# Kernel optimization log

Measured on AMD Instinct MI355X. Metric: run time of the kernel, lower is better.

The kernel has to match this reference:

```python
import jax, jax.numpy as jnp
import numpy as np


def gcn_layer(x, W, b, src, dst):
    """PyG GCNConv with improved=True: A_hat = A + 2I, D^-1/2 A_hat D^-1/2 X W + b."""
    n = x.shape[0]
    xw = x @ W  # [N, H]
    # degree counts each incoming edge (weight 1) plus self-loop weight 2
    deg = jnp.zeros((n,), x.dtype).at[dst].add(jnp.ones((src.shape[0],), x.dtype)) + 2.0
    dinv = jax.lax.rsqrt(deg)  # deg >= 2 always
    norm = (dinv[src] * dinv[dst])[:, None]  # [E, 1]
    agg = jax.ops.segment_sum(xw[src] * norm, dst, num_segments=n)  # scatter-add to dst
    agg = agg + (2.0 * dinv * dinv)[:, None] * xw  # self-loop contribution (weight 2)
    return agg + b


def xavier(k, shape):
    lim = (6.0 / (shape[0] + shape[1])) ** 0.5
    return jax.random.uniform(k, shape, jnp.float32, -lim, lim)


def setup_inputs() -> dict:
    key = jax.random.key(0)
    ks = jax.random.split(key, 8)
    N, E, D = 100_000, 1_600_000, 64  # nodes, edges, features_dim
    H1, H2 = 64, 64                   # gnn_dims
    M1, M2 = 128, 64                  # ind_pol_dims
    rep = jax.random.normal(ks[0], (N, D), jnp.float32)
    edge_index = jax.random.randint(ks[1], (2, E), 0, N, jnp.int32)
    return {
        "rep": rep,
        "edge_index": edge_index,
        "W1": xavier(ks[2], (D, H1)), "b1": jnp.zeros((H1,), jnp.float32),
        "W2": xavier(ks[3], (H1, H2)), "b2": jnp.zeros((H2,), jnp.float32),
        "Wa": xavier(ks[4], (H2 + D, M1)), "ba": jnp.zeros((M1,), jnp.float32),
        "Wb": xavier(ks[5], (M1, M2)), "bb": jnp.zeros((M2,), jnp.float32),
        "Wo": xavier(ks[6], (M2, 1)), "bo": jnp.zeros((1,), jnp.float32),
    }


def reference(rep, edge_index, W1, b1, W2, b2, Wa, ba, Wb, bb, Wo, bo):
    src, dst = edge_index[0], edge_index[1]
    # eval mode: f.dropout(training=False) is identity
    h = jax.nn.relu(gcn_layer(rep, W1, b1, src, dst))
    h = jax.nn.relu(gcn_layer(h, W2, b2, src, dst))
    z = jnp.concatenate([rep, h], axis=1)  # [N, D + H2]
    z = jax.nn.relu(z @ Wa + ba)
    z = jax.nn.relu(z @ Wb + bb)
    prob = jax.nn.sigmoid(z @ Wo + bo)[:, 0]  # [N]
    # gumbel_softmax(hard=True, tau=1) over logits = [1-p, p] (torch semantics:
    # probabilities fed directly as logits, as in the original code)
    logits = jnp.stack([1.0 - prob, prob], axis=1)  # [N, 2]
    u = jax.random.uniform(jax.random.key(42), logits.shape, jnp.float32, 1e-20, 1.0)
    g = -jnp.log(-jnp.log(u))
    y = jax.nn.softmax(logits + g, axis=1)
    hard = jax.nn.one_hot(jnp.argmax(y, axis=1), 2, dtype=y.dtype)
    st = hard + y - jax.lax.stop_gradient(y)  # straight-through
    ind = st @ jnp.array([[0.0], [1.0]], dtype=y.dtype)  # mm with [[0],[1]]
    return (prob, ind[:, 0])
```

## Files before the change

kernel.cpp:

```cpp
#include <hip/hip_runtime.h>
#include <math.h>


__device__ __forceinline__ unsigned rotl32(unsigned x, int r) {
  return (x << r) | (x >> (32 - r));
}

__device__ __forceinline__ void threefry2x32(unsigned k0, unsigned k1,
                                             unsigned x0, unsigned x1,
                                             unsigned& o0, unsigned& o1) {
  unsigned ks2 = k0 ^ k1 ^ 0x1BD11BDAu;
#define TF_RND(r) { x0 += x1; x1 = rotl32(x1, (r)); x1 ^= x0; }
  x0 += k0; x1 += k1;
  TF_RND(13) TF_RND(15) TF_RND(26) TF_RND(6)
  x0 += k1; x1 += ks2 + 1u;
  TF_RND(17) TF_RND(29) TF_RND(16) TF_RND(24)
  x0 += ks2; x1 += k0 + 2u;
  TF_RND(13) TF_RND(15) TF_RND(26) TF_RND(6)
  x0 += k0; x1 += k1 + 3u;
  TF_RND(17) TF_RND(29) TF_RND(16) TF_RND(24)
  x0 += k1; x1 += ks2 + 4u;
  TF_RND(13) TF_RND(15) TF_RND(26) TF_RND(6)
  x0 += ks2; x1 += k0 + 5u;
#undef TF_RND
  o0 = x0; o1 = x1;
}

__device__ __forceinline__ unsigned jax_random_bits_u32(unsigned k0, unsigned k1,
                                                        unsigned flat_idx) {
  unsigned a, b;
  threefry2x32(k0, k1, 0u, flat_idx, a, b);
  return a ^ b;
}

#define BSHIFT 8
#define BMASK 255

__global__ __launch_bounds__(256) void coarse_hist_kernel(
    const int* __restrict__ dst, int* __restrict__ coarse, int E) {
  __shared__ int h[512];
  for (int i = threadIdx.x; i < 512; i += 256) h[i] = 0;
  __syncthreads();
  for (int e = blockIdx.x * blockDim.x + threadIdx.x; e < E;
       e += gridDim.x * blockDim.x)
    atomicAdd(&h[dst[e] >> BSHIFT], 1);
  __syncthreads();
  for (int i = threadIdx.x; i < 512; i += 256)
    if (h[i]) atomicAdd(&coarse[i], h[i]);
}

__global__ __launch_bounds__(512) void coarse_scan_kernel(
    const int* __restrict__ coarse, int* __restrict__ bbase,
    int* __restrict__ cbase, int NBUCK) {
  __shared__ int sh[512];
  int t = threadIdx.x;
  int v = (t < NBUCK) ? coarse[t] : 0;
  sh[t] = v;
  __syncthreads();
  for (int o = 1; o < 512; o <<= 1) {
    int a = (t >= o) ? sh[t - o] : 0;
    __syncthreads();
    sh[t] += a;
    __syncthreads();
  }
  if (t < NBUCK) {
    int ex = sh[t] - v;
    bbase[t] = ex;
    cbase[t] = ex;
    if (t == NBUCK - 1) bbase[NBUCK] = sh[t];
  }
}

#define CHUNK 4096
__global__ __launch_bounds__(256) void scatter_gemm_kernel(
    const int* __restrict__ src, const int* __restrict__ dst,
    int* __restrict__ cbase, int* __restrict__ pkB, int E, int nbA,
    const float* __restrict__ X, const float* __restrict__ W,
    float* __restrict__ Y, int N) {
  __shared__ int smem[9216];
  const int t = threadIdx.x;

  if (blockIdx.x < nbA) {
    int* sS = smem;
    int* dS = smem + 4096;
    int* cnt = smem + 8192;
    int* base = smem + 8704;
    const int e0 = blockIdx.x * CHUNK;
    const int n = min(CHUNK, E - e0);
    for (int i = t; i < 512; i += 256) cnt[i] = 0;
    for (int i = t; i < n; i += 256) {
      sS[i] = src[e0 + i];
      dS[i] = dst[e0 + i];
    }
    __syncthreads();
    for (int i = t; i < n; i += 256) atomicAdd(&cnt[dS[i] >> BSHIFT], 1);
    __syncthreads();
    for (int i = t; i < 512; i += 256) {
      int c = cnt[i];
      base[i] = c ? atomicAdd(&cbase[i], c) : 0;
    }
    __syncthreads();
    for (int i = t; i < 512; i += 256) cnt[i] = 0;
    __syncthreads();
    for (int i = t; i < n; i += 256) {
      int d = dS[i];
      int b = d >> BSHIFT;
      int r = atomicAdd(&cnt[b], 1);
      pkB[base[b] + r] = ((d & BMASK) << 20) | sS[i];
    }
    return;
  }

  float* Ws = (float*)smem;
  float* Xs = (float*)smem + 4096;
  {
    const float4* W4 = (const float4*)W;
    float4* Ws4 = (float4*)Ws;
    for (int i = t; i < 1024; i += 256) Ws4[i] = W4[i];
  }
  const int row0 = (blockIdx.x - nbA) * 64;
  for (int i = t; i < 64 * 16; i += 256) {
    int r = i >> 4, c4 = i & 15;
    int gr = row0 + r;
    float4 v = make_float4(0.f, 0.f, 0.f, 0.f);
    if (gr < N) v = *(const float4*)&X[(size_t)gr * 64 + c4 * 4];
    *(float4*)&Xs[r * 68 + c4 * 4] = v;
  }
  __syncthreads();

  const int tx = t & 15, ty = t >> 4;
  const int c0 = tx * 4;
  const int r0 = ty * 4;
  float acc[4][4];
#pragma unroll
  for (int i = 0; i < 4; ++i)
#pragma unroll
    for (int j = 0; j < 4; ++j) acc[i][j] = 0.f;

#pragma unroll 4
  for (int k4 = 0; k4 < 16; ++k4) {
    float4 xv[4];
#pragma unroll
    for (int i = 0; i < 4; ++i)
      xv[i] = *(const float4*)&Xs[(r0 + i) * 68 + k4 * 4];
#pragma unroll
    for (int kk = 0; kk < 4; ++kk) {
      float w[4];
#pragma unroll
      for (int j = 0; j < 4; ++j) w[j] = Ws[(k4 * 4 + kk) * 64 + c0 + j];
      const float xk[4] = {
          kk == 0 ? xv[0].x : kk == 1 ? xv[0].y : kk == 2 ? xv[0].z : xv[0].w,
          kk == 0 ? xv[1].x : kk == 1 ? xv[1].y : kk == 2 ? xv[1].z : xv[1].w,
          kk == 0 ? xv[2].x : kk == 1 ? xv[2].y : kk == 2 ? xv[2].z : xv[2].w,
          kk == 0 ? xv[3].x : kk == 1 ? xv[3].y : kk == 2 ? xv[3].z : xv[3].w};
#pragma unroll
      for (int i = 0; i < 4; ++i)
#pragma unroll
        for (int j = 0; j < 4; ++j) acc[i][j] = fmaf(xk[i], w[j], acc[i][j]);
    }
  }

#pragma unroll
  for (int i = 0; i < 4; ++i) {
    int gr = row0 + r0 + i;
    if (gr >= N) continue;
    float4 v = make_float4(acc[i][0], acc[i][1], acc[i][2], acc[i][3]);
    *(float4*)&Y[(size_t)gr * 64 + c0] = v;
  }
}

__global__ __launch_bounds__(256) void bucket_finalize_kernel(
    const int* __restrict__ pkB, const int* __restrict__ bbase,
    int* __restrict__ off, float* __restrict__ dinv, int* __restrict__ srcS,
    int N) {
  __shared__ int cnt[256];
  __shared__ int sh[256];
  const int t = threadIdx.x;
  const int b = blockIdx.x;
  const int lo = bbase[b], hi = bbase[b + 1];
  cnt[t] = 0;
  __syncthreads();
  for (int i = lo + t; i < hi; i += 256) atomicAdd(&cnt[pkB[i] >> 20], 1);
  __syncthreads();
  const int deg = cnt[t];
  sh[t] = deg;
  __syncthreads();
  for (int o = 1; o < 256; o <<= 1) {
    int a = (t >= o) ? sh[t - o] : 0;
    __syncthreads();
    sh[t] += a;
    __syncthreads();
  }
  const int ex = sh[t] - deg;
  const int node = (b << BSHIFT) + t;
  if (node < N) {
    off[node] = lo + ex;
    dinv[node] = 1.0f / sqrtf((float)deg + 2.0f);
    if (node == N - 1) off[N] = hi;
  }
  cnt[t] = lo + ex;
  __syncthreads();
  for (int i = lo + t; i < hi; i += 256) {
    int u = pkB[i];
    int pos = atomicAdd(&cnt[u >> 20], 1);
    srcS[pos] = u & 0xFFFFF;
  }
}

__global__ __launch_bounds__(256) void aggregate_kernel(
    const float* __restrict__ xws, const int* __restrict__ srcS,
    const int* __restrict__ off, const float* __restrict__ dinv,
    const float* __restrict__ dinvS, const float* __restrict__ bias,
    float* __restrict__ h, int N) {
  int node = (blockIdx.x * blockDim.x + threadIdx.x) >> 6;
  int lane = threadIdx.x & 63;
  int g = lane >> 4;
  int fq = lane & 15;
  if (node >= N) return;
  const float4* xw4 = (const float4*)xws;
  int beg = off[node], end = off[node + 1];
  float4 a0 = make_float4(0.f, 0.f, 0.f, 0.f);
  float4 a1 = a0, a2 = a0, a3 = a0;
  if (dinvS) {
    for (int e = beg; e < end; e += 16) {
      int e0 = e + g, e1 = e + 4 + g, e2 = e + 8 + g, e3 = e + 12 + g;
      int s0 = srcS[min(e0, end - 1)];
      int s1 = srcS[min(e1, end - 1)];
      int s2 = srcS[min(e2, end - 1)];
      int s3 = srcS[min(e3, end - 1)];
      float d0 = dinvS[s0], d1 = dinvS[s1], d2 = dinvS[s2], d3 = dinvS[s3];
      float4 v0 = xw4[(size_t)s0 * 16 + fq];
      float4 v1 = xw4[(size_t)s1 * 16 + fq];
      float4 v2 = xw4[(size_t)s2 * 16 + fq];
      float4 v3 = xw4[(size_t)s3 * 16 + fq];
      if (e0 < end) { a0.x += d0*v0.x; a0.y += d0*v0.y; a0.z += d0*v0.z; a0.w += d0*v0.w; }
      if (e1 < end) { a1.x += d1*v1.x; a1.y += d1*v1.y; a1.z += d1*v1.z; a1.w += d1*v1.w; }
      if (e2 < end) { a2.x += d2*v2.x; a2.y += d2*v2.y; a2.z += d2*v2.z; a2.w += d2*v2.w; }
      if (e3 < end) { a3.x += d3*v3.x; a3.y += d3*v3.y; a3.z += d3*v3.z; a3.w += d3*v3.w; }
    }
  } else {
    for (int e = beg; e < end; e += 16) {
      int e0 = e + g, e1 = e + 4 + g, e2 = e + 8 + g, e3 = e + 12 + g;
      int s0 = srcS[min(e0, end - 1)];
      int s1 = srcS[min(e1, end - 1)];
      int s2 = srcS[min(e2, end - 1)];
      int s3 = srcS[min(e3, end - 1)];
      float4 v0 = xw4[(size_t)s0 * 16 + fq];
      float4 v1 = xw4[(size_t)s1 * 16 + fq];
      float4 v2 = xw4[(size_t)s2 * 16 + fq];
      float4 v3 = xw4[(size_t)s3 * 16 + fq];
      if (e0 < end) { a0.x += v0.x; a0.y += v0.y; a0.z += v0.z; a0.w += v0.w; }
      if (e1 < end) { a1.x += v1.x; a1.y += v1.y; a1.z += v1.z; a1.w += v1.w; }
      if (e2 < end) { a2.x += v2.x; a2.y += v2.y; a2.z += v2.z; a2.w += v2.w; }
      if (e3 < end) { a3.x += v3.x; a3.y += v3.y; a3.z += v3.z; a3.w += v3.w; }
    }
  }
  float4 a;
  a.x = (a0.x + a1.x) + (a2.x + a3.x);
  a.y = (a0.y + a1.y) + (a2.y + a3.y);
  a.z = (a0.z + a1.z) + (a2.z + a3.z);
  a.w = (a0.w + a1.w) + (a2.w + a3.w);
  a.x += __shfl_xor(a.x, 16, 64); a.x += __shfl_xor(a.x, 32, 64);
  a.y += __shfl_xor(a.y, 16, 64); a.y += __shfl_xor(a.y, 32, 64);
  a.z += __shfl_xor(a.z, 16, 64); a.z += __shfl_xor(a.z, 32, 64);
  a.w += __shfl_xor(a.w, 16, 64); a.w += __shfl_xor(a.w, 32, 64);
  if (g == 0) {
    float di = dinv[node];
    float4 self = xw4[(size_t)node * 16 + fq];
    if (dinvS) { self.x *= di; self.y *= di; self.z *= di; self.w *= di; }
    float4 b = ((const float4*)bias)[fq];
    float4 r;
    r.x = fmaxf(di * (a.x + 2.0f * self.x) + b.x, 0.f);
    r.y = fmaxf(di * (a.y + 2.0f * self.y) + b.y, 0.f);
    r.z = fmaxf(di * (a.z + 2.0f * self.z) + b.z, 0.f);
    r.w = fmaxf(di * (a.w + 2.0f * self.w) + b.w, 0.f);
    *(float4*)&h[(size_t)node * 64 + fq * 4] = r;
  }
}

__global__ __launch_bounds__(256) void gemm64v2_kernel(
    const float* __restrict__ X, const float* __restrict__ W,
    const float* __restrict__ dinv, float* __restrict__ Y, int N) {
  __shared__ float Ws[64 * 64];
  __shared__ float Xs[64 * 68];
  const int t = threadIdx.x;
  {
    const float4* W4 = (const float4*)W;
    float4* Ws4 = (float4*)Ws;
    for (int i = t; i < 16 * 64; i += 256) Ws4[i] = W4[i];
  }
  const int row0 = blockIdx.x * 64;
  for (int i = t; i < 64 * 16; i += 256) {
    int r = i >> 4, c4 = i & 15;
    int gr = row0 + r;
    float4 v = make_float4(0.f, 0.f, 0.f, 0.f);
    if (gr < N) v = *(const float4*)&X[(size_t)gr * 64 + c4 * 4];
    *(float4*)&Xs[r * 68 + c4 * 4] = v;
  }
  __syncthreads();

  const int tx = t & 15, ty = t >> 4;
  const int c0 = tx * 4;
  const int r0 = ty * 4;
  float acc[4][4];
#pragma unroll
  for (int i = 0; i < 4; ++i)
#pragma unroll
    for (int j = 0; j < 4; ++j) acc[i][j] = 0.f;

#pragma unroll 4
  for (int k4 = 0; k4 < 16; ++k4) {
    float4 xv[4];
#pragma unroll
    for (int i = 0; i < 4; ++i)
      xv[i] = *(const float4*)&Xs[(r0 + i) * 68 + k4 * 4];
#pragma unroll
    for (int kk = 0; kk < 4; ++kk) {
      float w[4];
#pragma unroll
      for (int j = 0; j < 4; ++j) w[j] = Ws[(k4 * 4 + kk) * 64 + c0 + j];
      const float xk[4] = {
          kk == 0 ? xv[0].x : kk == 1 ? xv[0].y : kk == 2 ? xv[0].z : xv[0].w,
          kk == 0 ? xv[1].x : kk == 1 ? xv[1].y : kk == 2 ? xv[1].z : xv[1].w,
          kk == 0 ? xv[2].x : kk == 1 ? xv[2].y : kk == 2 ? xv[2].z : xv[2].w,
          kk == 0 ? xv[3].x : kk == 1 ? xv[3].y : kk == 2 ? xv[3].z : xv[3].w};
#pragma unroll
      for (int i = 0; i < 4; ++i)
#pragma unroll
        for (int j = 0; j < 4; ++j) acc[i][j] = fmaf(xk[i], w[j], acc[i][j]);
    }
  }

#pragma unroll
  for (int i = 0; i < 4; ++i) {
    int gr = row0 + r0 + i;
    if (gr >= N) continue;
    float sc = dinv[gr];
    float4 v = make_float4(acc[i][0] * sc, acc[i][1] * sc, acc[i][2] * sc,
                           acc[i][3] * sc);
    *(float4*)&Y[(size_t)gr * 64 + c0] = v;
  }
}

__global__ __launch_bounds__(256) void head_mega_kernel(
    const float* __restrict__ rep, const float* __restrict__ h2,
    const float* __restrict__ Wa, const float* __restrict__ ba,
    const float* __restrict__ Wb, const float* __restrict__ bb,
    const float* __restrict__ Wo, const float* __restrict__ bo,
    float* __restrict__ out, int N) {
  __shared__ float Xs[64 * 128];
  __shared__ float Wbuf[32 * 128];
  const int t = threadIdx.x;
  const int row0 = blockIdx.x * 64;

  for (int i = t; i < 2048; i += 256) {
    int r = i >> 5, c4 = i & 31;
    int gr = row0 + r;
    float4 v = make_float4(0.f, 0.f, 0.f, 0.f);
    if (gr < N)
      v = (c4 < 16) ? *(const float4*)&rep[(size_t)gr * 64 + c4 * 4]
                    : *(const float4*)&h2[(size_t)gr * 64 + (c4 - 16) * 4];
    int scol = (c4 * 4 + ((r >> 2) << 2)) & 127;
    *(float4*)&Xs[r * 128 + scol] = v;
  }

  const int tx = t & 15, ty = t >> 4;
  const int cL = tx * 4;
  const int cH = 64 + tx * 4;
  const int r0 = ty * 4;
  float za[4][8];
#pragma unroll
  for (int i = 0; i < 4; ++i)
#pragma unroll
    for (int j = 0; j < 8; ++j) za[i][j] = 0.f;

  for (int chunk = 0; chunk < 4; ++chunk) {
    __syncthreads();
    const float4* Wa4 = (const float4*)(Wa + chunk * 32 * 128);
    float4* Wd = (float4*)Wbuf;
    for (int i = t; i < 1024; i += 256) Wd[i] = Wa4[i];
    __syncthreads();
    const int kb = chunk * 32;
#pragma unroll 2
    for (int kk = 0; kk < 32; ++kk) {
      const int kc = (kb + kk + (ty << 2)) & 127;
      float x[4];
#pragma unroll
      for (int i = 0; i < 4; ++i) x[i] = Xs[(r0 + i) * 128 + kc];
      float4 w0 = *(const float4*)&Wbuf[kk * 128 + cL];
      float4 w1 = *(const float4*)&Wbuf[kk * 128 + cH];
      const float w[8] = {w0.x, w0.y, w0.z, w0.w, w1.x, w1.y, w1.z, w1.w};
#pragma unroll
      for (int i = 0; i < 4; ++i)
#pragma unroll
        for (int j = 0; j < 8; ++j) za[i][j] = fmaf(x[i], w[j], za[i][j]);
    }
  }
#pragma unroll
  for (int i = 0; i < 4; ++i) {
#pragma unroll
    for (int j = 0; j < 4; ++j) {
      za[i][j] = fmaxf(za[i][j] + ba[cL + j], 0.f);
      za[i][4 + j] = fmaxf(za[i][4 + j] + ba[cH + j], 0.f);
    }
  }

  __syncthreads();
  float* zaS = Xs;
  {
    int sL = (cL + (ty << 2)) & 127;
    int sH = (cH + (ty << 2)) & 127;
#pragma unroll
    for (int i = 0; i < 4; ++i) {
      *(float4*)&zaS[(r0 + i) * 128 + sL] =
          make_float4(za[i][0], za[i][1], za[i][2], za[i][3]);
      *(float4*)&zaS[(r0 + i) * 128 + sH] =
          make_float4(za[i][4], za[i][5], za[i][6], za[i][7]);
    }
  }

  const int c0b = tx * 4;
  float zb[4][4];
#pragma unroll
  for (int i = 0; i < 4; ++i)
#pragma unroll
    for (int j = 0; j < 4; ++j) zb[i][j] = 0.f;

  for (int chunk = 0; chunk < 2; ++chunk) {
    __syncthreads();
    const float4* Wb4 = (const float4*)(Wb + chunk * 64 * 64);
    float4* Wd = (float4*)Wbuf;
    for (int i = t; i < 1024; i += 256) Wd[i] = Wb4[i];
    __syncthreads();
    const int kb = chunk * 64;
#pragma unroll 4
    for (int kk = 0; kk < 64; ++kk) {
      const int kc = (kb + kk + (ty << 2)) & 127;
      float x[4];
#pragma unroll
      for (int i = 0; i < 4; ++i) x[i] = zaS[(r0 + i) * 128 + kc];
      float4 w = *(const float4*)&Wbuf[kk * 64 + c0b];
      const float wj[4] = {w.x, w.y, w.z, w.w};
#pragma unroll
      for (int i = 0; i < 4; ++i)
#pragma unroll
        for (int j = 0; j < 4; ++j) zb[i][j] = fmaf(x[i], wj[j], zb[i][j]);
    }
  }
  float part[4];
#pragma unroll
  for (int i = 0; i < 4; ++i) {
    part[i] = 0.f;
#pragma unroll
    for (int j = 0; j < 4; ++j) {
      float v = fmaxf(zb[i][j] + bb[c0b + j], 0.f);
      part[i] = fmaf(v, Wo[c0b + j], part[i]);
    }
  }
  __syncthreads();
  float* red = Wbuf;
#pragma unroll
  for (int i = 0; i < 4; ++i) red[tx * 68 + r0 + i] = part[i];
  __syncthreads();
  if (t < 64) {
    int gr = row0 + t;
    if (gr < N) {
      float s = 0.f;
#pragma unroll
      for (int u = 0; u < 16; ++u) s += red[u * 68 + t];
      float w = s + bo[0];
      float p = 1.0f / (1.0f + expf(-w));
      unsigned i = (unsigned)gr;
      unsigned bits0 = jax_random_bits_u32(0u, 42u, 2u * i);
      unsigned bits1 = jax_random_bits_u32(0u, 42u, 2u * i + 1u);
      float f0 = __uint_as_float((bits0 >> 9) | 0x3f800000u) - 1.0f;
      float f1 = __uint_as_float((bits1 >> 9) | 0x3f800000u) - 1.0f;
      float u0 = fmaxf(1e-20f, f0 + 1e-20f);
      float u1 = fmaxf(1e-20f, f1 + 1e-20f);
      float g0 = -logf(-logf(u0));
      float g1 = -logf(-logf(u1));
      float a0 = (1.0f - p) + g0;
      float a1 = p + g1;
      float m = fmaxf(a0, a1);
      float e0 = expf(a0 - m), e1 = expf(a1 - m);
      float ssum = e0 + e1;
      float y0 = e0 / ssum, y1 = e1 / ssum;
      float hard1 = (y1 > y0) ? 1.0f : 0.0f;
      float st1 = (hard1 + y1) - y1;
      out[gr] = p;
      out[N + gr] = st1;
    }
  }
}

extern "C" void kernel_launch(void* const* d_in, const int* in_sizes, int n_in,
                              void* d_out, int out_size, void* d_ws, size_t ws_size,
                              hipStream_t stream) {
  const float* rep = (const float*)d_in[0];
  const int* ei = (const int*)d_in[1];
  const float* W1 = (const float*)d_in[2];
  const float* b1 = (const float*)d_in[3];
  const float* W2 = (const float*)d_in[4];
  const float* b2 = (const float*)d_in[5];
  const float* Wa = (const float*)d_in[6];
  const float* ba = (const float*)d_in[7];
  const float* Wb = (const float*)d_in[8];
  const float* bb = (const float*)d_in[9];
  const float* Wo = (const float*)d_in[10];
  const float* bo = (const float*)d_in[11];
  float* out = (float*)d_out;

  const int N = in_sizes[0] / 64;
  const int E = in_sizes[1] / 2;
  const int* srcI = ei;
  const int* dstI = ei + E;

  const int NBUCK = (N + 255) >> BSHIFT;

  float* ws = (float*)d_ws;
  float* bufA = ws;
  float* bufB = bufA + (size_t)N * 64;
  float* dinv = bufB + (size_t)N * 64;
  int* coarse = (int*)(dinv + N);
  int* bbase = coarse + 512;
  int* cbase = bbase + 513;
  int* off = cbase + 512;
  int* pkB = off + N + 1;
  int* srcS = pkB + E;

  const int nb64 = (N + 63) / 64;
  const int nbW = (N + 3) / 4;
  const int nbA = (E + CHUNK - 1) / CHUNK;

  hipMemsetAsync(coarse, 0, 512 * 4, stream);
  coarse_hist_kernel<<<256, 256, 0, stream>>>(dstI, coarse, E);
  coarse_scan_kernel<<<1, 512, 0, stream>>>(coarse, bbase, cbase, NBUCK);
  scatter_gemm_kernel<<<nbA + nb64, 256, 0, stream>>>(
      srcI, dstI, cbase, pkB, E, nbA, rep, W1, bufA, N);
  bucket_finalize_kernel<<<NBUCK, 256, 0, stream>>>(pkB, bbase, off, dinv,
                                                    srcS, N);

  aggregate_kernel<<<nbW, 256, 0, stream>>>(bufA, srcS, off, dinv, dinv, b1,
                                            bufB, N);

  gemm64v2_kernel<<<nb64, 256, 0, stream>>>(bufB, W2, dinv, bufA, N);
  aggregate_kernel<<<nbW, 256, 0, stream>>>(bufA, srcS, off, dinv, nullptr, b2,
                                            bufB, N);

  head_mega_kernel<<<nb64, 256, 0, stream>>>(rep, bufB, Wa, ba, Wb, bb, Wo, bo,
                                             out, N);
}
```

Before: 386.6 us.

## Double-buffer head MLP weight tiles with register prefetch in shared memory

Splits the Wa and Wb weight loads in the head kernel into smaller chunks held in a two-slot shared buffer. Each thread prefetches the next chunk into registers while the current chunk is being used in the FMA loop, which lets global loads overlap compute and drops one barrier per chunk. The reduction scratch moves to the Xs buffer, and the weight buffer shrinks from 16 KB to 8 KB of LDS, which may allow more resident blocks. The trade-off is more chunks and therefore more barriers in total, plus a few extra registers for the prefetch.

```diff
diff --git a/kernel.cpp b/kernel.cpp
--- a/kernel.cpp
+++ b/kernel.cpp
@@ -349,7 +349,7 @@
     const float* __restrict__ Wo, const float* __restrict__ bo,
     float* __restrict__ out, int N) {
   __shared__ float Xs[64 * 128];
-  __shared__ float Wbuf[32 * 128];
+  __shared__ float Wd[2][1024];
   const int t = threadIdx.x;
   const int row0 = blockIdx.x * 64;
 
@@ -374,28 +374,35 @@
 #pragma unroll
     for (int j = 0; j < 8; ++j) za[i][j] = 0.f;
 
-  for (int chunk = 0; chunk < 4; ++chunk) {
-    __syncthreads();
-    const float4* Wa4 = (const float4*)(Wa + chunk * 32 * 128);
-    float4* Wd = (float4*)Wbuf;
-    for (int i = t; i < 1024; i += 256) Wd[i] = Wa4[i];
-    __syncthreads();
-    const int kb = chunk * 32;
+  const float4* Wa4 = (const float4*)Wa;
+  {
+    float4 w0 = Wa4[t];
+    *(float4*)&Wd[0][t * 4] = w0;
+  }
+  __syncthreads();
+  for (int c = 0; c < 16; ++c) {
+    float4 wnext;
+    if (c + 1 < 16) wnext = Wa4[(c + 1) * 256 + t];
+    const float* Wcur = Wd[c & 1];
+    const int kb = c * 8;
 #pragma unroll 2
-    for (int kk = 0; kk < 32; ++kk) {
+    for (int kk = 0; kk < 8; ++kk) {
       const int kc = (kb + kk + (ty << 2)) & 127;
       float x[4];
 #pragma unroll
       for (int i = 0; i < 4; ++i) x[i] = Xs[(r0 + i) * 128 + kc];
-      float4 w0 = *(const float4*)&Wbuf[kk * 128 + cL];
-      float4 w1 = *(const float4*)&Wbuf[kk * 128 + cH];
+      float4 w0 = *(const float4*)&Wcur[kk * 128 + cL];
+      float4 w1 = *(const float4*)&Wcur[kk * 128 + cH];
       const float w[8] = {w0.x, w0.y, w0.z, w0.w, w1.x, w1.y, w1.z, w1.w};
 #pragma unroll
       for (int i = 0; i < 4; ++i)
 #pragma unroll
         for (int j = 0; j < 8; ++j) za[i][j] = fmaf(x[i], w[j], za[i][j]);
     }
-  }
+    if (c + 1 < 16) *(float4*)&Wd[(c + 1) & 1][t * 4] = wnext;
+    __syncthreads();
+  }
+
 #pragma unroll
   for (int i = 0; i < 4; ++i) {
 #pragma unroll
@@ -405,9 +412,11 @@
     }
   }
 
-  __syncthreads();
   float* zaS = Xs;
+  const float4* Wb4 = (const float4*)Wb;
   {
+    float4 wb0 = Wb4[t];
+    *(float4*)&Wd[0][t * 4] = wb0;
     int sL = (cL + (ty << 2)) & 127;
     int sH = (cH + (ty << 2)) & 127;
 #pragma unroll
@@ -418,6 +427,7 @@
           make_float4(za[i][4], za[i][5], za[i][6], za[i][7]);
     }
   }
+  __syncthreads();
 
   const int c0b = tx * 4;
   float zb[4][4];
@@ -426,27 +436,28 @@
 #pragma unroll
     for (int j = 0; j < 4; ++j) zb[i][j] = 0.f;
 
-  for (int chunk = 0; chunk < 2; ++chunk) {
-    __syncthreads();
-    const float4* Wb4 = (const float4*)(Wb + chunk * 64 * 64);
-    float4* Wd = (float4*)Wbuf;
-    for (int i = t; i < 1024; i += 256) Wd[i] = Wb4[i];
-    __syncthreads();
-    const int kb = chunk * 64;
+  for (int c = 0; c < 8; ++c) {
+    float4 wnext;
+    if (c + 1 < 8) wnext = Wb4[(c + 1) * 256 + t];
+    const float* Wcur = Wd[c & 1];
+    const int kb = c * 16;
 #pragma unroll 4
-    for (int kk = 0; kk < 64; ++kk) {
+    for (int kk = 0; kk < 16; ++kk) {
       const int kc = (kb + kk + (ty << 2)) & 127;
       float x[4];
 #pragma unroll
       for (int i = 0; i < 4; ++i) x[i] = zaS[(r0 + i) * 128 + kc];
-      float4 w = *(const float4*)&Wbuf[kk * 64 + c0b];
+      float4 w = *(const float4*)&Wcur[kk * 64 + c0b];
       const float wj[4] = {w.x, w.y, w.z, w.w};
 #pragma unroll
       for (int i = 0; i < 4; ++i)
 #pragma unroll
         for (int j = 0; j < 4; ++j) zb[i][j] = fmaf(x[i], wj[j], zb[i][j]);
     }
-  }
+    if (c + 1 < 8) *(float4*)&Wd[(c + 1) & 1][t * 4] = wnext;
+    __syncthreads();
+  }
+
   float part[4];
 #pragma unroll
   for (int i = 0; i < 4; ++i) {
@@ -457,8 +468,7 @@
       part[i] = fmaf(v, Wo[c0b + j], part[i]);
     }
   }
-  __syncthreads();
-  float* red = Wbuf;
+  float* red = Xs;
 #pragma unroll
   for (int i = 0; i < 4; ++i) red[tx * 68 + r0 + i] = part[i];
   __syncthreads();
```

Result: no change. 385.0 us (-0.4%).
